# Kernel optimization log

Hardware: AMD Instinct MI355X
Metric: run time of the kernel (lower is better)

The kernel has to match this reference:

```python
import jax, jax.numpy as jnp
import numpy as np

B, D, L, H, W, T = 256, 512, 32, 14, 14, 8


def _lin(x, w, b=None):
    y = x @ w.T
    return y if b is None else y + b


def _conv1x1(x, w, b):  # x: [B,C,H,W], w: [O,C], b: [O]
    return jnp.einsum('oc,bchw->bohw', w, x) + b[None, :, None, None]


def setup_inputs() -> dict:
    key = jax.random.key(0)
    ks = jax.random.split(key, 24)
    s = 0.02
    inp = {
        'c': jax.random.normal(ks[0], (B, D), jnp.float32),
        'm': jax.random.normal(ks[1], (B, D), jnp.float32),
        'k': jax.random.normal(ks[2], (B, D, H, W), jnp.float32),
        'q': jax.random.normal(ks[3], (B, D), jnp.float32),
        'cw': jax.random.normal(ks[4], (B, L, D), jnp.float32),
        'mask': jax.random.randint(ks[5], (B, L), 0, 2, jnp.int32),
        'cs': jax.random.normal(ks[6], (T, B, D), jnp.float32),
        'ms': jax.random.normal(ks[7], (T, B, D), jnp.float32),
        # ControlUnit params
        'Wcq': jax.random.normal(ks[8], (D, 2 * D), jnp.float32) * s,
        'bcq': jnp.zeros((D,), jnp.float32),
        'Wca': jax.random.normal(ks[9], (1, D), jnp.float32) * s,
        'bca': jnp.zeros((1,), jnp.float32),
        # ReadUnit params
        'Wm_r': jax.random.normal(ks[10], (D, D), jnp.float32) * s,
        'bm_r': jnp.zeros((D,), jnp.float32),
        'Wk': jax.random.normal(ks[11], (D, D), jnp.float32) * s,
        'bk': jnp.zeros((D,), jnp.float32),
        'WI': jax.random.normal(ks[12], (D, 2 * D), jnp.float32) * s,
        'bI': jnp.zeros((D,), jnp.float32),
        'Wra': jax.random.normal(ks[13], (D, D), jnp.float32) * s,
        'bra': jnp.zeros((D,), jnp.float32),
        # WriteUnit params
        'Wm_w': jax.random.normal(ks[14], (D, 2 * D), jnp.float32) * s,
        'bm_w': jnp.zeros((D,), jnp.float32),
        'Wsa': jax.random.normal(ks[15], (1, D), jnp.float32) * s,
        'bsa': jnp.zeros((1,), jnp.float32),
        'Wm2': jax.random.normal(ks[16], (D, D), jnp.float32) * s,
        'bm2': jnp.zeros((D,), jnp.float32),
        'Wc': jax.random.normal(ks[17], (1, D), jnp.float32) * s,
        'bc': jnp.ones((1,), jnp.float32),  # linear_c.bias.data.fill_(1)
        'Ws': jax.random.normal(ks[18], (D, D), jnp.float32) * s,
    }
    return inp


def reference(c, m, k, q, cw, mask, cs, ms,
              Wcq, bcq, Wca, bca,
              Wm_r, bm_r, Wk, bk, WI, bI, Wra, bra,
              Wm_w, bm_w, Wsa, bsa, Wm2, bm2, Wc, bc, Ws):
    # ---- ControlUnit ----
    cq = _lin(jnp.concatenate([c, q], axis=1), Wcq, bcq)          # [B,D]
    ca = _lin(cq[:, None, :] * cw, Wca, bca)                      # [B,L,1]
    ca = jnp.where(mask[:, :, None] > 0, ca, -jnp.inf)            # mask padding
    cv = jax.nn.softmax(ca, axis=1)                               # [B,L,1]
    c_new = jnp.sum(cv * cw, axis=1)                              # [B,D]

    # ---- ReadUnit ----
    mI = _lin(m, Wm_r, bm_r)                                      # [B,D]
    I = mI[:, :, None, None] * _conv1x1(k, Wk, bk)                # [B,D,H,W]
    I_ = _conv1x1(jnp.concatenate([I, k], axis=1), WI, bI)        # [B,D,H,W]
    ra = _conv1x1(I_ * c_new[:, :, None, None], Wra, bra)         # [B,D,H,W]
    rv = jax.nn.softmax(ra, axis=1)                               # Softmax2d = over channels
    r = jnp.sum(rv * k, axis=(-1, -2))                            # [B,D]

    # ---- WriteUnit ----
    m_prev = _lin(jnp.concatenate([r, m], axis=1), Wm_w, bm_w)    # [B,D]
    m_ = _lin(m_prev, Wm2, bm2)                                   # [B,D]
    gate = jax.nn.sigmoid(_lin(c_new, Wc, bc))                    # [B,1]
    sa = jax.nn.softmax(_lin(cs * gate[None, :, :], Wsa, bsa), axis=0)  # [T,B,1]
    m_sa = jnp.sum(sa * ms, axis=0)                               # [B,D]
    m_ = m_ + m_sa @ Ws.T
    m_new = gate * m + (1.0 - gate) * m_                          # [B,D]

    return (c_new, m_new, cv, rv)
```

## Files before the change

kernel.cpp:

```cpp
#include <hip/hip_runtime.h>
#include <hip/hip_bf16.h>

#define BB 256
#define DD 512
#define LL 32
#define HWN 196
#define TT 8

typedef __hip_bfloat16 bf16;
typedef __attribute__((ext_vector_type(8))) short short8;
typedef __attribute__((ext_vector_type(4))) float f32x4;

__device__ __forceinline__ float b2f(bf16 x) { return __bfloat162float(x); }
__device__ __forceinline__ bf16 f2b(float x) { return __float2bfloat16(x); }
__device__ __forceinline__ unsigned short f2bu(float x) {
    bf16 h = __float2bfloat16(x);
    return *(unsigned short*)&h;
}
#define NEG_INF (-__builtin_huge_valf())

__global__ __launch_bounds__(256) void cvt_w_kernel(
    const float* __restrict__ src, unsigned short* __restrict__ dst, int n4)
{
    int i = blockIdx.x*256 + threadIdx.x;
    if (i < n4) {
        float4 f = ((const float4*)src)[i];
        ushort4 u;
        u.x = f2bu(f.x); u.y = f2bu(f.y); u.z = f2bu(f.z); u.w = f2bu(f.w);
        ((ushort4*)dst)[i] = u;
    }
}

__global__ __launch_bounds__(256) void small_gemm_kernel(
    const float* __restrict__ A1, int K1,
    const float* __restrict__ A2, int K2,
    const float* __restrict__ Wt, const float* __restrict__ bias,
    float* __restrict__ outf, int Dout)
{
    __shared__ float xs[1024];
    int b = blockIdx.x, tid = threadIdx.x;
    int K = K1 + K2;
    for (int i = tid; i < K; i += 256) {
        xs[i] = (i < K1) ? A1[(size_t)b*K1 + i] : A2[(size_t)b*K2 + (i - K1)];
    }
    __syncthreads();
    for (int d = tid; d < Dout; d += 256) {
        const float4* wrow = (const float4*)(Wt + (size_t)d * K);
        float acc = 0.f;
        for (int j = 0; j < K/4; ++j) {
            float4 w = wrow[j];
            acc += w.x*xs[j*4] + w.y*xs[j*4+1] + w.z*xs[j*4+2] + w.w*xs[j*4+3];
        }
        if (bias) acc += bias[d];
        outf[(size_t)b*Dout + d] = acc;
    }
}

__global__ __launch_bounds__(256) void control_kernel(
    const float* __restrict__ cq, const float* __restrict__ cw,
    const float* __restrict__ Wca, const float* __restrict__ bca,
    const int* __restrict__ mask,
    float* __restrict__ cnew_f, float* __restrict__ cv_out, float* __restrict__ cnew_out)
{
    __shared__ float u[DD];
    __shared__ float cas[LL];
    __shared__ float cvs[LL];
    int b = blockIdx.x, tid = threadIdx.x;
    for (int d = tid; d < DD; d += 256) u[d] = cq[(size_t)b*DD + d] * Wca[d];
    __syncthreads();
    int wave = tid >> 6, lane = tid & 63;
    float bca0 = bca[0];
    for (int lw = 0; lw < 8; ++lw) {
        int l = wave*8 + lw;
        const float4* w4 = (const float4*)(cw + ((size_t)(b*LL + l))*DD + lane*8);
        float4 wa = w4[0], wb = w4[1];
        const float* uu = &u[lane*8];
        float p = wa.x*uu[0] + wa.y*uu[1] + wa.z*uu[2] + wa.w*uu[3]
                + wb.x*uu[4] + wb.y*uu[5] + wb.z*uu[6] + wb.w*uu[7];
        for (int off = 32; off > 0; off >>= 1) p += __shfl_down(p, off);
        if (lane == 0) {
            float v = p + bca0;
            if (mask[b*LL + l] <= 0) v = NEG_INF;
            cas[l] = v;
        }
    }
    __syncthreads();
    if (tid < LL) {
        float mx = NEG_INF;
        for (int j = 0; j < LL; ++j) mx = fmaxf(mx, cas[j]);
        float s = 0.f;
        for (int j = 0; j < LL; ++j) s += __expf(cas[j] - mx);
        float cv = __expf(cas[tid] - mx) / s;
        cvs[tid] = cv;
        cv_out[b*LL + tid] = cv;
    }
    __syncthreads();
    for (int d = tid; d < DD; d += 256) {
        float acc = 0.f;
        for (int l = 0; l < LL; ++l) acc += cvs[l] * cw[((size_t)(b*LL + l))*DD + d];
        cnew_f[(size_t)b*DD + d] = acc;
        cnew_out[(size_t)b*DD + d] = acc;
    }
}

__device__ __forceinline__ void load4rows(const void* X, int isf32, size_t row, int n4, ushort4 r[4]) {
    if (isf32) {
        const float* p = (const float*)X + row*HWN + n4*4;
        #pragma unroll
        for (int i = 0; i < 4; ++i) {
            float4 f = *(const float4*)(p + (size_t)i*HWN);
            r[i].x = f2bu(f.x); r[i].y = f2bu(f.y); r[i].z = f2bu(f.z); r[i].w = f2bu(f.w);
        }
    } else {
        const unsigned short* p = (const unsigned short*)X + row*HWN + n4*4;
        #pragma unroll
        for (int i = 0; i < 4; ++i) r[i] = *(const ushort4*)(p + (size_t)i*HWN);
    }
}

__global__ __launch_bounds__(256) void conv_mfma_kernel(
    const void* __restrict__ X1, int x1f32, int C1,
    const void* __restrict__ X2, int x2f32,
    const unsigned short* __restrict__ Wb, int C,
    const float* __restrict__ bias, const float* __restrict__ oscale,
    unsigned short* __restrict__ Y)
{
    __shared__ __align__(16) uint2 Xs[8*212];
    int b = blockIdx.y, ot = blockIdx.x;
    int tid = threadIdx.x;
    int wave = tid >> 6, lane = tid & 63;
    int wm = wave >> 1, wn = wave & 1;
    int obase = ot*128 + wm*64;
    int n0 = wn*96;
    int ln = lane & 15, lq = lane >> 4;
    int C2 = C - C1;

    f32x4 acc[4][7];
    #pragma unroll
    for (int mt = 0; mt < 4; ++mt)
        #pragma unroll
        for (int nt = 0; nt < 7; ++nt) acc[mt][nt] = (f32x4){0.f, 0.f, 0.f, 0.f};

    for (int c0 = 0; c0 < C; c0 += 32) {
        __syncthreads();
        for (int idx = tid; idx < 8*49; idx += 256) {
            int n4 = idx % 49, kq = idx / 49;
            int c = c0 + kq*4;
            ushort4 r[4];
            if (c < C1) load4rows(X1, x1f32, (size_t)b*C1 + c, n4, r);
            else        load4rows(X2, x2f32, (size_t)b*C2 + (c - C1), n4, r);
            uint2* cell = &Xs[kq*212 + n4*4];
            *(uint4*)(cell) = make_uint4(
                (uint)r[0].x | ((uint)r[1].x << 16), (uint)r[2].x | ((uint)r[3].x << 16),
                (uint)r[0].y | ((uint)r[1].y << 16), (uint)r[2].y | ((uint)r[3].y << 16));
            *(uint4*)(cell + 2) = make_uint4(
                (uint)r[0].z | ((uint)r[1].z << 16), (uint)r[2].z | ((uint)r[3].z << 16),
                (uint)r[0].w | ((uint)r[1].w << 16), (uint)r[2].w | ((uint)r[3].w << 16));
        }
        __syncthreads();
        short8 a[4];
        #pragma unroll
        for (int mt = 0; mt < 4; ++mt)
            a[mt] = *(const short8*)(Wb + (size_t)(obase + mt*16 + ln)*C + c0 + lq*8);
        #pragma unroll
        for (int nt = 0; nt < 7; ++nt) {
            int n = n0 + nt*16 + ln;
            uint2 b0 = Xs[(lq*2)*212 + n];
            uint2 b1 = Xs[(lq*2 + 1)*212 + n];
            union { uint4 u; short8 s; } bb;
            bb.u = make_uint4(b0.x, b0.y, b1.x, b1.y);
            #pragma unroll
            for (int mt = 0; mt < 4; ++mt)
                acc[mt][nt] = __builtin_amdgcn_mfma_f32_16x16x32_bf16(a[mt], bb.s, acc[mt][nt], 0, 0, 0);
        }
    }
    #pragma unroll
    for (int mt = 0; mt < 4; ++mt) {
        #pragma unroll
        for (int rr = 0; rr < 4; ++rr) {
            int o = obase + mt*16 + lq*4 + rr;
            float bo = bias[o];
            float os = oscale ? oscale[(size_t)b*DD + o] : 1.f;
            #pragma unroll
            for (int nt = 0; nt < 7; ++nt) {
                int hw = n0 + nt*16 + ln;
                if (hw < HWN) {
                    float v = (acc[mt][nt][rr] + bo) * os;
                    Y[((size_t)b*DD + o)*HWN + hw] = f2bu(v);
                }
            }
        }
    }
}

__global__ __launch_bounds__(512) void softmax_r_kernel(
    const bf16* __restrict__ ra, const float* __restrict__ kin,
    float* __restrict__ rv, float* __restrict__ r)
{
    __shared__ float pm[2][HWN], ps[2][HWN];
    __shared__ float mxs[HWN], sis[HWN];
    int b = blockIdx.x, tid = threadIdx.x;
    int half = tid >> 8, hw = tid & 255;
    if (hw < HWN) {
        float m = NEG_INF, s = 0.f;
        const bf16* base = ra + ((size_t)b*DD + half*256)*HWN + hw;
        for (int c = 0; c < 256; ++c) {
            float x = b2f(base[(size_t)c*HWN]);
            float nm = fmaxf(m, x);
            s = s*__expf(m - nm) + __expf(x - nm);
            m = nm;
        }
        pm[half][hw] = m; ps[half][hw] = s;
    }
    __syncthreads();
    if (tid < HWN) {
        float m0 = pm[0][tid], m1 = pm[1][tid];
        float m = fmaxf(m0, m1);
        float s = ps[0][tid]*__expf(m0 - m) + ps[1][tid]*__expf(m1 - m);
        mxs[tid] = m; sis[tid] = 1.f/s;
    }
    __syncthreads();
    int wave = tid >> 6, lane = tid & 63;
    for (int ci = 0; ci < 64; ++ci) {
        int c = wave*64 + ci;
        float psum = 0.f;
        #pragma unroll
        for (int g = 0; g < 4; ++g) {
            int hw2 = lane + 64*g;
            if (hw2 < HWN) {
                size_t idx = ((size_t)b*DD + c)*HWN + hw2;
                float e = __expf(b2f(ra[idx]) - mxs[hw2]) * sis[hw2];
                rv[idx] = e;
                psum += e * kin[idx];
            }
        }
        for (int off = 32; off > 0; off >>= 1) psum += __shfl_down(psum, off);
        if (lane == 0) r[(size_t)b*DD + c] = psum;
    }
}

__global__ __launch_bounds__(64) void gate_kernel(
    const float* __restrict__ cnew, const float* __restrict__ Wc, const float* __restrict__ bc,
    float* __restrict__ gate)
{
    int b = blockIdx.x, lane = threadIdx.x;
    const float4* w4 = (const float4*)(Wc + lane*8);
    const float* x = &cnew[(size_t)b*DD + lane*8];
    float4 wa = w4[0], wb = w4[1];
    float p = wa.x*x[0] + wa.y*x[1] + wa.z*x[2] + wa.w*x[3]
            + wb.x*x[4] + wb.y*x[5] + wb.z*x[6] + wb.w*x[7];
    for (int off = 32; off > 0; off >>= 1) p += __shfl_down(p, off);
    if (lane == 0) gate[b] = 1.f / (1.f + __expf(-(p + bc[0])));
}

__global__ __launch_bounds__(256) void samsa_kernel(
    const float* __restrict__ cs, const float* __restrict__ ms,
    const float* __restrict__ Wsa, const float* __restrict__ bsa,
    const float* __restrict__ gate, float* __restrict__ msa)
{
    __shared__ float lg[TT];
    __shared__ float sas[TT];
    __shared__ float xw[DD];
    int b = blockIdx.x, tid = threadIdx.x;
    int wave = tid >> 6, lane = tid & 63;
    for (int d = tid; d < DD; d += 256) xw[d] = Wsa[d];
    __syncthreads();
    for (int tw = 0; tw < 2; ++tw) {
        int t = wave + 4*tw;
        const float4* c4 = (const float4*)(cs + ((size_t)t*BB + b)*DD + lane*8);
        float4 ca = c4[0], cb = c4[1];
        const float* ww = &xw[lane*8];
        float p = ca.x*ww[0] + ca.y*ww[1] + ca.z*ww[2] + ca.w*ww[3]
                + cb.x*ww[4] + cb.y*ww[5] + cb.z*ww[6] + cb.w*ww[7];
        for (int off = 32; off > 0; off >>= 1) p += __shfl_down(p, off);
        if (lane == 0) lg[t] = gate[b]*p + bsa[0];
    }
    __syncthreads();
    if (tid < TT) {
        float mx = NEG_INF;
        for (int j = 0; j < TT; ++j) mx = fmaxf(mx, lg[j]);
        float s = 0.f;
        for (int j = 0; j < TT; ++j) s += __expf(lg[j] - mx);
        sas[tid] = __expf(lg[tid] - mx) / s;
    }
    __syncthreads();
    for (int d = tid; d < DD; d += 256) {
        float acc = 0.f;
        for (int t = 0; t < TT; ++t) acc += sas[t] * ms[((size_t)t*BB + b)*DD + d];
        msa[(size_t)b*DD + d] = acc;
    }
}

__global__ __launch_bounds__(256) void final_kernel(
    const float* __restrict__ m, const float* __restrict__ gate,
    const float* __restrict__ mund, const float* __restrict__ msaw,
    float* __restrict__ mnew)
{
    int idx = blockIdx.x*256 + threadIdx.x;
    int b = idx >> 9;
    float g = gate[b];
    float mm = m[idx], mu = mund[idx], mw = msaw[idx];
    mnew[idx] = g * mm + (1.f - g) * (mu + mw);
}

extern "C" void kernel_launch(void* const* d_in, const int* in_sizes, int n_in,
                              void* d_out, int out_size, void* d_ws, size_t ws_size,
                              hipStream_t stream)
{
    (void)in_sizes; (void)n_in; (void)out_size; (void)ws_size;
    const float* c    = (const float*)d_in[0];
    const float* m    = (const float*)d_in[1];
    const float* k    = (const float*)d_in[2];
    const float* q    = (const float*)d_in[3];
    const float* cw   = (const float*)d_in[4];
    const int*   mask = (const int*)  d_in[5];
    const float* cs   = (const float*)d_in[6];
    const float* ms   = (const float*)d_in[7];
    const float* Wcq  = (const float*)d_in[8];
    const float* bcq  = (const float*)d_in[9];
    const float* Wca  = (const float*)d_in[10];
    const float* bca  = (const float*)d_in[11];
    const float* Wm_r = (const float*)d_in[12];
    const float* bm_r = (const float*)d_in[13];
    const float* Wk   = (const float*)d_in[14];
    const float* bk   = (const float*)d_in[15];
    const float* WI   = (const float*)d_in[16];
    const float* bI   = (const float*)d_in[17];
    const float* Wra  = (const float*)d_in[18];
    const float* bra  = (const float*)d_in[19];
    const float* Wm_w = (const float*)d_in[20];
    const float* bm_w = (const float*)d_in[21];
    const float* Wsa  = (const float*)d_in[22];
    const float* bsa  = (const float*)d_in[23];
    const float* Wm2  = (const float*)d_in[24];
    const float* bm2  = (const float*)d_in[25];
    const float* Wc   = (const float*)d_in[26];
    const float* bc   = (const float*)d_in[27];
    const float* Ws   = (const float*)d_in[28];

    float* out_cnew = (float*)d_out;
    float* out_mnew = out_cnew + BB*DD;
    float* out_cv   = out_mnew + BB*DD;
    float* out_rv   = out_cv + BB*LL;

    unsigned short* I_w  = (unsigned short*)out_rv;
    unsigned short* I2_w = (unsigned short*)((char*)out_rv + 51380224);

    char* w = (char*)d_ws;
    float* s0      = (float*)(w + 0);
    float* s1      = (float*)(w + 524288);
    float* s2      = (float*)(w + 1048576);
    float* s3      = (float*)(w + 1572864);
    unsigned short* Wkb  = (unsigned short*)(w + 2097152);
    unsigned short* WIb  = (unsigned short*)(w + 2621440);
    unsigned short* Wrab = (unsigned short*)(w + 3670016);
    unsigned short* ra_w = (unsigned short*)(w + 4194304);
    float* gate_w  = (float*)(w + 55574528);

    float* cq_w   = s0;
    float* r_w    = s0;
    float* cnew_w = s1;
    float* mI_w   = s2;
    float* mund_w = s2;
    float* mprev_w= s3;
    float* msa_w  = s3;
    float* msaw_w = out_mnew;

    cvt_w_kernel<<<256, 256, 0, stream>>>(Wk,  Wkb,  65536);
    cvt_w_kernel<<<512, 256, 0, stream>>>(WI,  WIb,  131072);
    cvt_w_kernel<<<256, 256, 0, stream>>>(Wra, Wrab, 65536);

    small_gemm_kernel<<<BB, 256, 0, stream>>>(c, DD, q, DD, Wcq, bcq, cq_w, DD);
    small_gemm_kernel<<<BB, 256, 0, stream>>>(m, DD, nullptr, 0, Wm_r, bm_r, mI_w, DD);
    control_kernel<<<BB, 256, 0, stream>>>(cq_w, cw, Wca, bca, mask, cnew_w, out_cv, out_cnew);

    conv_mfma_kernel<<<dim3(4, BB), 256, 0, stream>>>(k,    1, DD, nullptr, 0, Wkb,  DD,   bk,  mI_w,   I_w);
    conv_mfma_kernel<<<dim3(4, BB), 256, 0, stream>>>(I_w,  0, DD, k,       1, WIb,  2*DD, bI,  cnew_w, I2_w);
    conv_mfma_kernel<<<dim3(4, BB), 256, 0, stream>>>(I2_w, 0, DD, nullptr, 0, Wrab, DD,   bra, nullptr, ra_w);
    softmax_r_kernel<<<BB, 512, 0, stream>>>((const bf16*)ra_w, k, out_rv, r_w);

    small_gemm_kernel<<<BB, 256, 0, stream>>>(r_w, DD, m, DD, Wm_w, bm_w, mprev_w, DD);
    small_gemm_kernel<<<BB, 256, 0, stream>>>(mprev_w, DD, nullptr, 0, Wm2, bm2, mund_w, DD);
    gate_kernel<<<BB, 64, 0, stream>>>(cnew_w, Wc, bc, gate_w);
    samsa_kernel<<<BB, 256, 0, stream>>>(cs, ms, Wsa, bsa, gate_w, msa_w);
    small_gemm_kernel<<<BB, 256, 0, stream>>>(msa_w, DD, nullptr, 0, Ws, nullptr, msaw_w, DD);
    final_kernel<<<BB*DD/256, 256, 0, stream>>>(m, gate_w, mund_w, msaw_w, out_mnew);
}
```

Before: 906.7 us.

## Double-buffer conv MFMA tiles, rebalance N split, fuse gate and write-unit kernels

The conv MFMA kernel now double-buffers the LDS input tile and prefetches the next weight fragments and input rows into registers while the current tile is being multiplied, so only one barrier is needed per K step. Waves split the 196 spatial columns as 7+6 tiles instead of 7+7, which removes wasted padded MFMAs. The grid is transposed so adjacent blocks share the same weight tile. The gate computation is folded into the samsa kernel, and the Ws GEMV is fused with the final blend, removing two launches. In exchange the kernel uses more registers and twice the LDS, and the fused GEMV reads Ws row-wise per thread, which may coalesce poorly.

```diff
diff --git a/kernel.cpp b/kernel.cpp
--- a/kernel.cpp
+++ b/kernel.cpp
@@ -103,20 +103,7 @@
     }
 }
 
-__device__ __forceinline__ void load4rows(const void* X, int isf32, size_t row, int n4, ushort4 r[4]) {
-    if (isf32) {
-        const float* p = (const float*)X + row*HWN + n4*4;
-        #pragma unroll
-        for (int i = 0; i < 4; ++i) {
-            float4 f = *(const float4*)(p + (size_t)i*HWN);
-            r[i].x = f2bu(f.x); r[i].y = f2bu(f.y); r[i].z = f2bu(f.z); r[i].w = f2bu(f.w);
-        }
-    } else {
-        const unsigned short* p = (const unsigned short*)X + row*HWN + n4*4;
-        #pragma unroll
-        for (int i = 0; i < 4; ++i) r[i] = *(const ushort4*)(p + (size_t)i*HWN);
-    }
-}
+typedef union { float4 f4[4]; ushort4 u4[4]; } LCell;
 
 __global__ __launch_bounds__(256) void conv_mfma_kernel(
     const void* __restrict__ X1, int x1f32, int C1,
@@ -125,15 +112,70 @@
     const float* __restrict__ bias, const float* __restrict__ oscale,
     unsigned short* __restrict__ Y)
 {
-    __shared__ __align__(16) uint2 Xs[8*212];
-    int b = blockIdx.y, ot = blockIdx.x;
+    __shared__ __align__(16) uint2 Xs[2][8*212];
+    int b = blockIdx.x, ot = blockIdx.y;
     int tid = threadIdx.x;
     int wave = tid >> 6, lane = tid & 63;
     int wm = wave >> 1, wn = wave & 1;
     int obase = ot*128 + wm*64;
-    int n0 = wn*96;
+    int n0 = wn*112;
+    int ntn = wn ? 6 : 7;
     int ln = lane & 15, lq = lane >> 4;
     int C2 = C - C1;
+
+    int idx1 = tid + 256;
+    int n4_0 = tid % 49,  kq_0 = tid / 49;
+    int n4_1 = idx1 % 49, kq_1 = idx1 / 49;
+    bool v1 = idx1 < 8*49;
+
+    LCell preA, preB;
+
+    auto LOADC = [&](LCell& pc, int c0, int kq, int n4) {
+        int c = c0 + kq*4;
+        if (c < C1) {
+            if (x1f32) {
+                const float* p = (const float*)X1 + ((size_t)b*C1 + c)*HWN + n4*4;
+                #pragma unroll
+                for (int i = 0; i < 4; ++i) pc.f4[i] = *(const float4*)(p + (size_t)i*HWN);
+            } else {
+                const unsigned short* p = (const unsigned short*)X1 + ((size_t)b*C1 + c)*HWN + n4*4;
+                #pragma unroll
+                for (int i = 0; i < 4; ++i) pc.u4[i] = *(const ushort4*)(p + (size_t)i*HWN);
+            }
+        } else {
+            if (x2f32) {
+                const float* p = (const float*)X2 + ((size_t)b*C2 + (c - C1))*HWN + n4*4;
+                #pragma unroll
+                for (int i = 0; i < 4; ++i) pc.f4[i] = *(const float4*)(p + (size_t)i*HWN);
+            } else {
+                const unsigned short* p = (const unsigned short*)X2 + ((size_t)b*C2 + (c - C1))*HWN + n4*4;
+                #pragma unroll
+                for (int i = 0; i < 4; ++i) pc.u4[i] = *(const ushort4*)(p + (size_t)i*HWN);
+            }
+        }
+    };
+    auto PACKC = [&](LCell& pc, int c0, int kq, int n4, int buf) {
+        int c = c0 + kq*4;
+        int isf = (c < C1) ? x1f32 : x2f32;
+        ushort4 r[4];
+        if (isf) {
+            #pragma unroll
+            for (int i = 0; i < 4; ++i) {
+                float4 f = pc.f4[i];
+                r[i].x = f2bu(f.x); r[i].y = f2bu(f.y); r[i].z = f2bu(f.z); r[i].w = f2bu(f.w);
+            }
+        } else {
+            #pragma unroll
+            for (int i = 0; i < 4; ++i) r[i] = pc.u4[i];
+        }
+        uint2* cell = &Xs[buf][kq*212 + n4*4];
+        *(uint4*)(cell) = make_uint4(
+            (uint)r[0].x | ((uint)r[1].x << 16), (uint)r[2].x | ((uint)r[3].x << 16),
+            (uint)r[0].y | ((uint)r[1].y << 16), (uint)r[2].y | ((uint)r[3].y << 16));
+        *(uint4*)(cell + 2) = make_uint4(
+            (uint)r[0].z | ((uint)r[1].z << 16), (uint)r[2].z | ((uint)r[3].z << 16),
+            (uint)r[0].w | ((uint)r[1].w << 16), (uint)r[2].w | ((uint)r[3].w << 16));
+    };
 
     f32x4 acc[4][7];
     #pragma unroll
@@ -141,39 +183,51 @@
         #pragma unroll
         for (int nt = 0; nt < 7; ++nt) acc[mt][nt] = (f32x4){0.f, 0.f, 0.f, 0.f};
 
-    for (int c0 = 0; c0 < C; c0 += 32) {
-        __syncthreads();
-        for (int idx = tid; idx < 8*49; idx += 256) {
-            int n4 = idx % 49, kq = idx / 49;
-            int c = c0 + kq*4;
-            ushort4 r[4];
-            if (c < C1) load4rows(X1, x1f32, (size_t)b*C1 + c, n4, r);
-            else        load4rows(X2, x2f32, (size_t)b*C2 + (c - C1), n4, r);
-            uint2* cell = &Xs[kq*212 + n4*4];
-            *(uint4*)(cell) = make_uint4(
-                (uint)r[0].x | ((uint)r[1].x << 16), (uint)r[2].x | ((uint)r[3].x << 16),
-                (uint)r[0].y | ((uint)r[1].y << 16), (uint)r[2].y | ((uint)r[3].y << 16));
-            *(uint4*)(cell + 2) = make_uint4(
-                (uint)r[0].z | ((uint)r[1].z << 16), (uint)r[2].z | ((uint)r[3].z << 16),
-                (uint)r[0].w | ((uint)r[1].w << 16), (uint)r[2].w | ((uint)r[3].w << 16));
-        }
-        __syncthreads();
-        short8 a[4];
-        #pragma unroll
-        for (int mt = 0; mt < 4; ++mt)
-            a[mt] = *(const short8*)(Wb + (size_t)(obase + mt*16 + ln)*C + c0 + lq*8);
+    short8 a_cur[4], a_nxt[4];
+    #pragma unroll
+    for (int mt = 0; mt < 4; ++mt)
+        a_cur[mt] = *(const short8*)(Wb + (size_t)(obase + mt*16 + ln)*C + 0 + lq*8);
+
+    LOADC(preA, 0, kq_0, n4_0);
+    if (v1) LOADC(preB, 0, kq_1, n4_1);
+    PACKC(preA, 0, kq_0, n4_0, 0);
+    if (v1) PACKC(preB, 0, kq_1, n4_1, 0);
+    __syncthreads();
+
+    int nsteps = C/32;
+    for (int s = 0; s < nsteps; ++s) {
+        int buf = s & 1;
+        int c0 = s*32;
+        bool more = (s + 1 < nsteps);
+        if (more) {
+            #pragma unroll
+            for (int mt = 0; mt < 4; ++mt)
+                a_nxt[mt] = *(const short8*)(Wb + (size_t)(obase + mt*16 + ln)*C + (c0+32) + lq*8);
+            LOADC(preA, c0+32, kq_0, n4_0);
+            if (v1) LOADC(preB, c0+32, kq_1, n4_1);
+        }
         #pragma unroll
         for (int nt = 0; nt < 7; ++nt) {
-            int n = n0 + nt*16 + ln;
-            uint2 b0 = Xs[(lq*2)*212 + n];
-            uint2 b1 = Xs[(lq*2 + 1)*212 + n];
-            union { uint4 u; short8 s; } bb;
-            bb.u = make_uint4(b0.x, b0.y, b1.x, b1.y);
+            if (nt < ntn) {
+                int n = n0 + nt*16 + ln;
+                uint2 b0 = Xs[buf][(lq*2)*212 + n];
+                uint2 b1 = Xs[buf][(lq*2 + 1)*212 + n];
+                union { uint4 u; short8 s8; } bb;
+                bb.u = make_uint4(b0.x, b0.y, b1.x, b1.y);
+                #pragma unroll
+                for (int mt = 0; mt < 4; ++mt)
+                    acc[mt][nt] = __builtin_amdgcn_mfma_f32_16x16x32_bf16(a_cur[mt], bb.s8, acc[mt][nt], 0, 0, 0);
+            }
+        }
+        if (more) {
+            PACKC(preA, c0+32, kq_0, n4_0, buf^1);
+            if (v1) PACKC(preB, c0+32, kq_1, n4_1, buf^1);
             #pragma unroll
-            for (int mt = 0; mt < 4; ++mt)
-                acc[mt][nt] = __builtin_amdgcn_mfma_f32_16x16x32_bf16(a[mt], bb.s, acc[mt][nt], 0, 0, 0);
-        }
-    }
+            for (int mt = 0; mt < 4; ++mt) a_cur[mt] = a_nxt[mt];
+        }
+        __syncthreads();
+    }
+
     #pragma unroll
     for (int mt = 0; mt < 4; ++mt) {
         #pragma unroll
@@ -239,28 +293,16 @@
     }
 }
 
-__global__ __launch_bounds__(64) void gate_kernel(
-    const float* __restrict__ cnew, const float* __restrict__ Wc, const float* __restrict__ bc,
-    float* __restrict__ gate)
-{
-    int b = blockIdx.x, lane = threadIdx.x;
-    const float4* w4 = (const float4*)(Wc + lane*8);
-    const float* x = &cnew[(size_t)b*DD + lane*8];
-    float4 wa = w4[0], wb = w4[1];
-    float p = wa.x*x[0] + wa.y*x[1] + wa.z*x[2] + wa.w*x[3]
-            + wb.x*x[4] + wb.y*x[5] + wb.z*x[6] + wb.w*x[7];
-    for (int off = 32; off > 0; off >>= 1) p += __shfl_down(p, off);
-    if (lane == 0) gate[b] = 1.f / (1.f + __expf(-(p + bc[0])));
-}
-
 __global__ __launch_bounds__(256) void samsa_kernel(
     const float* __restrict__ cs, const float* __restrict__ ms,
     const float* __restrict__ Wsa, const float* __restrict__ bsa,
-    const float* __restrict__ gate, float* __restrict__ msa)
+    const float* __restrict__ cnew, const float* __restrict__ Wc, const float* __restrict__ bc,
+    float* __restrict__ gate_out, float* __restrict__ msa)
 {
     __shared__ float lg[TT];
     __shared__ float sas[TT];
     __shared__ float xw[DD];
+    __shared__ float gsh;
     int b = blockIdx.x, tid = threadIdx.x;
     int wave = tid >> 6, lane = tid & 63;
     for (int d = tid; d < DD; d += 256) xw[d] = Wsa[d];
@@ -273,15 +315,28 @@
         float p = ca.x*ww[0] + ca.y*ww[1] + ca.z*ww[2] + ca.w*ww[3]
                 + cb.x*ww[4] + cb.y*ww[5] + cb.z*ww[6] + cb.w*ww[7];
         for (int off = 32; off > 0; off >>= 1) p += __shfl_down(p, off);
-        if (lane == 0) lg[t] = gate[b]*p + bsa[0];
+        if (lane == 0) lg[t] = p;
+    }
+    if (wave == 0) {
+        const float4* w4 = (const float4*)(Wc + lane*8);
+        const float* x = &cnew[(size_t)b*DD + lane*8];
+        float4 wa = w4[0], wb = w4[1];
+        float p = wa.x*x[0] + wa.y*x[1] + wa.z*x[2] + wa.w*x[3]
+                + wb.x*x[4] + wb.y*x[5] + wb.z*x[6] + wb.w*x[7];
+        for (int off = 32; off > 0; off >>= 1) p += __shfl_down(p, off);
+        if (lane == 0) {
+            float g = 1.f / (1.f + __expf(-(p + bc[0])));
+            gsh = g; gate_out[b] = g;
+        }
     }
     __syncthreads();
     if (tid < TT) {
+        float g = gsh, b0 = bsa[0];
         float mx = NEG_INF;
-        for (int j = 0; j < TT; ++j) mx = fmaxf(mx, lg[j]);
+        for (int j = 0; j < TT; ++j) mx = fmaxf(mx, g*lg[j] + b0);
         float s = 0.f;
-        for (int j = 0; j < TT; ++j) s += __expf(lg[j] - mx);
-        sas[tid] = __expf(lg[tid] - mx) / s;
+        for (int j = 0; j < TT; ++j) s += __expf(g*lg[j] + b0 - mx);
+        sas[tid] = __expf(g*lg[tid] + b0 - mx) / s;
     }
     __syncthreads();
     for (int d = tid; d < DD; d += 256) {
@@ -291,16 +346,26 @@
     }
 }
 
-__global__ __launch_bounds__(256) void final_kernel(
+__global__ __launch_bounds__(256) void write_final_kernel(
+    const float* __restrict__ msa, const float* __restrict__ Ws,
     const float* __restrict__ m, const float* __restrict__ gate,
-    const float* __restrict__ mund, const float* __restrict__ msaw,
-    float* __restrict__ mnew)
-{
-    int idx = blockIdx.x*256 + threadIdx.x;
-    int b = idx >> 9;
+    const float* __restrict__ mund, float* __restrict__ mnew)
+{
+    __shared__ float xs[DD];
+    int b = blockIdx.x, tid = threadIdx.x;
+    for (int i = tid; i < DD; i += 256) xs[i] = msa[(size_t)b*DD + i];
+    __syncthreads();
     float g = gate[b];
-    float mm = m[idx], mu = mund[idx], mw = msaw[idx];
-    mnew[idx] = g * mm + (1.f - g) * (mu + mw);
+    for (int d = tid; d < DD; d += 256) {
+        const float4* wrow = (const float4*)(Ws + (size_t)d * DD);
+        float acc = 0.f;
+        for (int j = 0; j < DD/4; ++j) {
+            float4 w = wrow[j];
+            acc += w.x*xs[j*4] + w.y*xs[j*4+1] + w.z*xs[j*4+2] + w.w*xs[j*4+3];
+        }
+        size_t idx = (size_t)b*DD + d;
+        mnew[idx] = g * m[idx] + (1.f - g) * (mund[idx] + acc);
+    }
 }
 
 extern "C" void kernel_launch(void* const* d_in, const int* in_sizes, int n_in,
@@ -364,7 +429,6 @@
     float* mund_w = s2;
     float* mprev_w= s3;
     float* msa_w  = s3;
-    float* msaw_w = out_mnew;
 
     cvt_w_kernel<<<256, 256, 0, stream>>>(Wk,  Wkb,  65536);
     cvt_w_kernel<<<512, 256, 0, stream>>>(WI,  WIb,  131072);
@@ -374,15 +438,13 @@
     small_gemm_kernel<<<BB, 256, 0, stream>>>(m, DD, nullptr, 0, Wm_r, bm_r, mI_w, DD);
     control_kernel<<<BB, 256, 0, stream>>>(cq_w, cw, Wca, bca, mask, cnew_w, out_cv, out_cnew);
 
-    conv_mfma_kernel<<<dim3(4, BB), 256, 0, stream>>>(k,    1, DD, nullptr, 0, Wkb,  DD,   bk,  mI_w,   I_w);
-    conv_mfma_kernel<<<dim3(4, BB), 256, 0, stream>>>(I_w,  0, DD, k,       1, WIb,  2*DD, bI,  cnew_w, I2_w);
-    conv_mfma_kernel<<<dim3(4, BB), 256, 0, stream>>>(I2_w, 0, DD, nullptr, 0, Wrab, DD,   bra, nullptr, ra_w);
+    conv_mfma_kernel<<<dim3(BB, 4), 256, 0, stream>>>(k,    1, DD, nullptr, 0, Wkb,  DD,   bk,  mI_w,   I_w);
+    conv_mfma_kernel<<<dim3(BB, 4), 256, 0, stream>>>(I_w,  0, DD, k,       1, WIb,  2*DD, bI,  cnew_w, I2_w);
+    conv_mfma_kernel<<<dim3(BB, 4), 256, 0, stream>>>(I2_w, 0, DD, nullptr, 0, Wrab, DD,   bra, nullptr, ra_w);
     softmax_r_kernel<<<BB, 512, 0, stream>>>((const bf16*)ra_w, k, out_rv, r_w);
 
     small_gemm_kernel<<<BB, 256, 0, stream>>>(r_w, DD, m, DD, Wm_w, bm_w, mprev_w, DD);
     small_gemm_kernel<<<BB, 256, 0, stream>>>(mprev_w, DD, nullptr, 0, Wm2, bm2, mund_w, DD);
-    gate_kernel<<<BB, 64, 0, stream>>>(cnew_w, Wc, bc, gate_w);
-    samsa_kernel<<<BB, 256, 0, stream>>>(cs, ms, Wsa, bsa, gate_w, msa_w);
-    small_gemm_kernel<<<BB, 256, 0, stream>>>(msa_w, DD, nullptr, 0, Ws, nullptr, msaw_w, DD);
-    final_kernel<<<BB*DD/256, 256, 0, stream>>>(m, gate_w, mund_w, msaw_w, out_mnew);
-}
+    samsa_kernel<<<BB, 256, 0, stream>>>(cs, ms, Wsa, bsa, cnew_w, Wc, bc, gate_w, msa_w);
+    write_final_kernel<<<BB, 256, 0, stream>>>(msa_w, Ws, m, gate_w, mund_w, out_mnew);
+}
```

Result: slower. 1.162 ms (+28.2%).
